# Kernel optimization log

Measured on AMD Instinct MI355X. Metric: run time of the kernel, lower is better.

The kernel has to match this reference:

```python
import jax, jax.numpy as jnp
import numpy as np

HEADS, DIM_HEAD, LANDMARKS, PINV_ITERS = 8, 64, 256, 6
CONV_K = 33  # nystrom residual depthwise conv kernel


def _pinv(x, iters):
    # Moore-Penrose iterative pseudo-inverse (lucidrains nystrom-attention)
    ax = jnp.abs(x)
    denom = ax.sum(-1).max() * ax.sum(-2).max()
    z = jnp.swapaxes(x, -1, -2) / denom
    I = jnp.eye(x.shape[-1], dtype=x.dtype)
    for _ in range(iters):
        xz = x @ z
        z = 0.25 * z @ (13.0 * I - xz @ (15.0 * I - xz @ (7.0 * I - xz)))
    return z


def _nystrom(x, qkv_w, out_w, out_b, conv_w):
    b, n, _ = x.shape
    m = LANDMARKS
    pad = (m - n % m) % m
    x = jnp.pad(x, ((0, 0), (pad, 0), (0, 0)))  # pad at front, as in reference impl
    npad = n + pad
    qkv = x @ qkv_w  # (b, npad, 3*h*dh), no bias
    q, k, v = jnp.split(qkv, 3, axis=-1)
    heads = lambda t: t.reshape(b, npad, HEADS, DIM_HEAD).transpose(0, 2, 1, 3)  # bhnd
    q, k, v = heads(q), heads(k), heads(v)
    q = q * (DIM_HEAD ** -0.5)
    l = npad // m
    q_l = q.reshape(b, HEADS, m, l, DIM_HEAD).mean(3)  # (b,h,m,dh) landmarks
    k_l = k.reshape(b, HEADS, m, l, DIM_HEAD).mean(3)
    attn1 = jax.nn.softmax(jnp.einsum('bhid,bhjd->bhij', q, k_l), -1)    # (b,h,npad,m)
    attn2 = jax.nn.softmax(jnp.einsum('bhid,bhjd->bhij', q_l, k_l), -1)  # (b,h,m,m)
    attn3 = jax.nn.softmax(jnp.einsum('bhid,bhjd->bhij', q_l, k), -1)    # (b,h,m,npad)
    out = (attn1 @ _pinv(attn2, PINV_ITERS)) @ (attn3 @ v)               # (b,h,npad,dh)
    # residual depthwise conv along sequence dim (groups=heads)
    res = jax.lax.conv_general_dilated(
        v, conv_w, (1, 1), ((CONV_K // 2, CONV_K // 2), (0, 0)),
        dimension_numbers=('NCHW', 'OIHW', 'NCHW'), feature_group_count=HEADS)
    out = out + res
    out = out.transpose(0, 2, 1, 3).reshape(b, npad, HEADS * DIM_HEAD)
    out = out @ out_w + out_b
    return out[:, -n:]  # drop front padding


def setup_inputs() -> dict:
    key = jax.random.key(0)
    ks = jax.random.split(key, 12)
    N, D, E, WP = 30000, 1024, 480000, 256
    inner = HEADS * DIM_HEAD
    s = lambda k, shape, fan: jax.random.normal(k, shape, jnp.float32) * (fan ** -0.5)
    return {
        'dense': jax.random.normal(ks[0], (1, N, D), jnp.float32),
        'edge_index': jax.random.randint(ks[1], (2, E), 0, N),
        'adj_vals': jax.random.uniform(ks[2], (E,), jnp.float32),
        'qkv_w': s(ks[3], (D, 3 * inner), D),
        'out_w': s(ks[4], (inner, D), inner),
        'out_b': jnp.zeros((D,), jnp.float32),
        'conv_w': s(ks[5], (HEADS, 1, CONV_K, 1), CONV_K),
        'wq_w': s(ks[6], (D, WP), D),
        'wq_b': jnp.zeros((WP,), jnp.float32),
        'wk_w': s(ks[7], (D, WP), D),
        'wk_b': jnp.zeros((WP,), jnp.float32),
        'wv_w': s(ks[8], (D, D), D),
        'wv_b': jnp.zeros((D,), jnp.float32),
    }


def reference(dense, edge_index, adj_vals, qkv_w, out_w, out_b, conv_w,
              wq_w, wq_b, wk_w, wk_b, wv_w, wv_b):
    n = dense.shape[1]
    enc = _nystrom(dense, qkv_w, out_w, out_b, conv_w)  # (1, n, D)
    encoder_output = enc[0] + dense                     # (1, n, D), broadcast as in torch
    x = encoder_output[0]                               # (n, D)
    # CustomAttention: per-edge dot-product scores
    q = x @ wq_w + wq_b                                 # (n, 256)
    k = x @ wk_w + wk_b
    scores = jnp.sum(q[edge_index[0]] * k[edge_index[1]], axis=-1) / jnp.sqrt(jnp.float32(q.shape[-1]))
    # NeighborAggregator: elementwise sparse mult by adjacency values, row-sum, global softmax
    A_raw = jax.ops.segment_sum(scores * adj_vals, edge_index[0], num_segments=n)  # (n,)
    norm_alpha = jax.nn.softmax(A_raw)
    value = dense @ wv_w + wv_b                         # (1, n, D)
    xl = norm_alpha[:, None] * value                    # (1, n, D)
    sw = jax.nn.sigmoid(-xl) ** 2
    xo = xl * 2.0 * sw + 2.0 * encoder_output * (1.0 - sw)
    return xo, A_raw
```

## Files before the change

### kernel.cpp

```cpp
#include <hip/hip_runtime.h>

#define NSEQ   30000
#define NPAD   30208
#define FPAD   208
#define DMODEL 1024
#define NHEAD  8
#define DHEAD  64
#define LM     256
#define LCHUNK 118
#define INNER  512
#define NCHUNK 59

typedef long long ll;
typedef unsigned short us;
typedef unsigned int uint32;
typedef __attribute__((ext_vector_type(8))) __bf16 bf16x8;
typedef __attribute__((ext_vector_type(4))) float f32x4;

__device__ __forceinline__ float b2f(us u) {
    union { unsigned int i; float f; } x; x.i = ((unsigned int)u) << 16; return x.f;
}
__device__ __forceinline__ us f2b(float f) {
    union { float f; unsigned int i; } x; x.f = f;
    unsigned int r = x.i + 0x7fffu + ((x.i >> 16) & 1u);
    return (us)(r >> 16);
}
__device__ __forceinline__ void gload16(const us* g, us* l) {
    __builtin_amdgcn_global_load_lds(
        (__attribute__((address_space(1))) void*)(const_cast<us*>(g)),
        (__attribute__((address_space(3))) void*)l, 16, 0, 0);
}

template<int EPI>
__global__ __launch_bounds__(256)
void bgemm(const us* __restrict__ A, const us* __restrict__ Bt,
           float* __restrict__ C, us* __restrict__ C2,
           const float* __restrict__ bias, const float* __restrict__ addp,
           int Mm, int Nn, int Kk, int lda, int ldb, int ldc, int ldadd,
           int Mstore, int Nstore, int rSub)
{
    __shared__ us As[2][128 * 32];
    __shared__ us Bs[2][128 * 32];

    int nwg = gridDim.x * gridDim.y;
    int orig = blockIdx.y * gridDim.x + blockIdx.x;
    int qd = nwg >> 3, rm = nwg & 7;
    int xcd = orig & 7, off = orig >> 3;
    int swz = (xcd < rm ? xcd * (qd + 1) : rm * (qd + 1) + (xcd - rm) * qd) + off;
    int by = swz / gridDim.x, bx = swz - by * gridDim.x;
    int m0 = by * 128, n0 = bx * 128;

    int tid = threadIdx.x, w = tid >> 6, lane = tid & 63;
    int wr = w >> 1, wc = w & 1;
    int nkt = Kk >> 5;

    int q0 = w * 128;
    int qa0 = q0 + lane, qa1 = q0 + 64 + lane;
    int r0s = qa0 >> 2, c0s = (qa0 & 3) ^ ((r0s >> 1) & 3);
    int r1s = qa1 >> 2, c1s = (qa1 & 3) ^ ((r1s >> 1) & 3);
    int ar0 = m0 + r0s; if (ar0 > Mm - 1) ar0 = Mm - 1;
    int ar1 = m0 + r1s; if (ar1 > Mm - 1) ar1 = Mm - 1;
    int br0 = n0 + r0s; if (br0 > Nn - 1) br0 = Nn - 1;
    int br1 = n0 + r1s; if (br1 > Nn - 1) br1 = Nn - 1;
    const us* pa0 = A + (ll)ar0 * lda + c0s * 8;
    const us* pa1 = A + (ll)ar1 * lda + c1s * 8;
    const us* pb0 = Bt + (ll)br0 * ldb + c0s * 8;
    const us* pb1 = Bt + (ll)br1 * ldb + c1s * 8;
    int la0o = q0 * 8, la1o = (q0 + 64) * 8;

    int l15 = lane & 15, l4 = lane >> 4;
    int aoff[4], boff[4];
#pragma unroll
    for (int f = 0; f < 4; f++) {
        int row = wr * 64 + f * 16 + l15;
        aoff[f] = row * 32 + ((l4 ^ ((row >> 1) & 3)) << 3);
        int col = wc * 64 + f * 16 + l15;
        boff[f] = col * 32 + ((l4 ^ ((col >> 1) & 3)) << 3);
    }

    f32x4 acc[4][4];
#pragma unroll
    for (int i = 0; i < 4; i++)
#pragma unroll
        for (int j = 0; j < 4; j++) acc[i][j] = (f32x4){0.f, 0.f, 0.f, 0.f};

    auto stage = [&](int buf, int kt) {
        int k0 = kt << 5;
        gload16(pa0 + k0, &As[buf][la0o]);
        gload16(pa1 + k0, &As[buf][la1o]);
        gload16(pb0 + k0, &Bs[buf][la0o]);
        gload16(pb1 + k0, &Bs[buf][la1o]);
    };

    stage(0, 0);
    for (int kt = 0; kt < nkt; ++kt) {
        int cur = kt & 1;
        if (kt + 1 < nkt) {
            stage(cur ^ 1, kt + 1);
            asm volatile("s_waitcnt vmcnt(4)" ::: "memory");
        } else {
            asm volatile("s_waitcnt vmcnt(0)" ::: "memory");
        }
        __builtin_amdgcn_s_barrier();
        asm volatile("" ::: "memory");
        bf16x8 af[4], bfr[4];
#pragma unroll
        for (int f = 0; f < 4; f++) af[f] = *(const bf16x8*)&As[cur][aoff[f]];
#pragma unroll
        for (int f = 0; f < 4; f++) bfr[f] = *(const bf16x8*)&Bs[cur][boff[f]];
#pragma unroll
        for (int i = 0; i < 4; i++)
#pragma unroll
            for (int j = 0; j < 4; j++)
                acc[i][j] = __builtin_amdgcn_mfma_f32_16x16x32_bf16(af[i], bfr[j], acc[i][j], 0, 0, 0);
        asm volatile("" ::: "memory");
        __builtin_amdgcn_s_barrier();
        asm volatile("" ::: "memory");
    }

#pragma unroll
    for (int fm = 0; fm < 4; fm++) {
        int rb = m0 + wr * 64 + fm * 16 + l4 * 4;
#pragma unroll
        for (int fn = 0; fn < 4; fn++) {
            int c = n0 + wc * 64 + fn * 16 + l15;
            if (c >= Nstore) continue;
#pragma unroll
            for (int i = 0; i < 4; i++) {
                int r = rb + i - rSub;
                if (r < 0 || r >= Mstore) continue;
                float v = acc[fm][fn][i];
                if (EPI == 3) {
                    int part = c >> 9, hh = (c >> 6) & 7, dd = c & 63;
                    float o = (part == 0) ? v * 0.125f : v;
                    C2[((ll)(part * 8 + hh) * NPAD + r) * 64 + dd] = f2b(o);
                } else if (EPI == 10) {
                    C2[(ll)r * ldc + c] = f2b(v + bias[c]);
                } else if (EPI == 12) {
                    C2[(ll)r * ldc + c] = f2b(v + bias[c] + addp[(ll)r * ldadd + c]);
                }
            }
        }
    }
}

__global__ __launch_bounds__(512)
void mega1(const us* __restrict__ XN, us* __restrict__ ZN, us* __restrict__ ZT,
           us* __restrict__ ZN2, us* __restrict__ ZT2,
           us* __restrict__ Y, us* __restrict__ W1T, us* __restrict__ W2T,
           us* __restrict__ W3T,
           const us* __restrict__ QLB, const us* __restrict__ Kh,
           const us* __restrict__ VT, us* __restrict__ KVPb, float* __restrict__ ZP,
           const us* __restrict__ Vh, const float* __restrict__ cw,
           us* __restrict__ ATTP,
           const us* __restrict__ DENSEP, const us* __restrict__ WVT,
           const float* __restrict__ wvb, us* __restrict__ VALB,
           const us* __restrict__ Qh, const us* __restrict__ KLB,
           us* __restrict__ P1)
{
    __shared__ us LDSu[24576];
    int b = blockIdx.x;
    int tid = threadIdx.x, w = tid >> 6, lane = tid & 63;
    int l15 = lane & 15, l4 = lane >> 4;

    if (b < 8) {
        __builtin_amdgcn_s_setprio(1);
        ll hb = (ll)b << 16;
        int wr = w >> 2, wc = w & 3;
        int sra = tid >> 2, sca = ((tid & 3) ^ ((sra >> 1) & 3)) * 8;
        int q1 = tid + 512;
        int srb1 = q1 >> 2, scb1 = ((q1 & 3) ^ ((srb1 >> 1) & 3)) * 8;
        int aoff[4], boff[4];
#pragma unroll
        for (int f = 0; f < 4; f++) {
            int row = wr * 64 + f * 16 + l15;
            aoff[f] = row * 32 + ((l4 ^ ((row >> 1) & 3)) << 3);
            int col = wc * 64 + f * 16 + l15;
            boff[f] = 4096 + col * 32 + ((l4 ^ ((col >> 1) & 3)) << 3);
        }
        f32x4 acc[4][4];
        auto gemmS = [&](const us* Ah, const us* Bt) {
#pragma unroll
            for (int i = 0; i < 4; i++)
#pragma unroll
                for (int j = 0; j < 4; j++) acc[i][j] = (f32x4){0.f, 0.f, 0.f, 0.f};
            const us* pa  = Ah + (ll)sra * 256 + sca;
            const us* pb0 = Bt + (ll)sra * 256 + sca;
            const us* pb1 = Bt + (ll)srb1 * 256 + scb1;
            auto stg = [&](int buf, int kt) {
                int k0 = kt << 5;
                gload16(pa + k0, &LDSu[buf + tid * 8]);
                gload16(pb0 + k0, &LDSu[buf + 4096 + tid * 8]);
                gload16(pb1 + k0, &LDSu[buf + 8192 + tid * 8]);
            };
            stg(0, 0);
            for (int kt = 0; kt < 8; ++kt) {
                int buf = (kt & 1) * 12288;
                if (kt < 7) {
                    stg(buf ^ 12288, kt + 1);
                    asm volatile("s_waitcnt vmcnt(3)" ::: "memory");
                } else {
                    asm volatile("s_waitcnt vmcnt(0)" ::: "memory");
                }
                __builtin_amdgcn_s_barrier();
                asm volatile("" ::: "memory");
                bf16x8 af[4], bfr[4];
#pragma unroll
                for (int f = 0; f < 4; f++) af[f] = *(const bf16x8*)&LDSu[buf + aoff[f]];
#pragma unroll
                for (int f = 0; f < 4; f++) bfr[f] = *(const bf16x8*)&LDSu[buf + boff[f]];
#pragma unroll
                for (int i = 0; i < 4; i++)
#pragma unroll
                    for (int j = 0; j < 4; j++)
                        acc[i][j] = __builtin_amdgcn_mfma_f32_16x16x32_bf16(af[i], bfr[j], acc[i][j], 0, 0, 0);
                asm volatile("" ::: "memory");
                __builtin_amdgcn_s_barrier();
                asm volatile("" ::: "memory");
            }
        };

        us* znc = ZN; us* ztc = ZT; us* znn = ZN2; us* ztn = ZT2;
        for (int it = 0; it < 6; ++it) {
#pragma unroll
            for (int hf = 0; hf < 2; ++hf) {
                gemmS(XN + hb + hf * 32768, ztc + hb);
#pragma unroll
                for (int fm = 0; fm < 4; fm++) {
                    int rb = hf * 128 + wr * 64 + fm * 16 + l4 * 4;
#pragma unroll
                    for (int fn = 0; fn < 4; fn++) {
                        int c = wc * 64 + fn * 16 + l15;
                        ushort4 u;
#pragma unroll
                        for (int i = 0; i < 4; i++) {
                            float v = acc[fm][fn][i];
                            Y[hb + (ll)(rb + i) * 256 + c] = f2b(v);
                            ((us*)&u)[i] = f2b(((rb + i == c) ? 7.0f : 0.0f) - v);
                        }
                        *(ushort4*)&W1T[hb + (ll)c * 256 + rb] = u;
                    }
                }
            }
            __syncthreads();
#pragma unroll
            for (int hf = 0; hf < 2; ++hf) {
                gemmS(Y + hb + hf * 32768, W1T + hb);
#pragma unroll
                for (int fm = 0; fm < 4; fm++) {
                    int rb = hf * 128 + wr * 64 + fm * 16 + l4 * 4;
#pragma unroll
                    for (int fn = 0; fn < 4; fn++) {
                        int c = wc * 64 + fn * 16 + l15;
                        ushort4 u;
#pragma unroll
                        for (int i = 0; i < 4; i++)
                            ((us*)&u)[i] = f2b(((rb + i == c) ? 15.0f : 0.0f) - acc[fm][fn][i]);
                        *(ushort4*)&W2T[hb + (ll)c * 256 + rb] = u;
                    }
                }
            }
            __syncthreads();
#pragma unroll
            for (int hf = 0; hf < 2; ++hf) {
                gemmS(Y + hb + hf * 32768, W2T + hb);
#pragma unroll
                for (int fm = 0; fm < 4; fm++) {
                    int rb = hf * 128 + wr * 64 + fm * 16 + l4 * 4;
#pragma unroll
                    for (int fn = 0; fn < 4; fn++) {
                        int c = wc * 64 + fn * 16 + l15;
                        ushort4 u;
#pragma unroll
                        for (int i = 0; i < 4; i++)
                            ((us*)&u)[i] = f2b(((rb + i == c) ? 13.0f : 0.0f) - acc[fm][fn][i]);
                        *(ushort4*)&W3T[hb + (ll)c * 256 + rb] = u;
                    }
                }
            }
            __syncthreads();
#pragma unroll
            for (int hf = 0; hf < 2; ++hf) {
                gemmS(znc + hb + hf * 32768, W3T + hb);
#pragma unroll
                for (int fm = 0; fm < 4; fm++) {
                    int rb = hf * 128 + wr * 64 + fm * 16 + l4 * 4;
#pragma unroll
                    for (int fn = 0; fn < 4; fn++) {
                        int c = wc * 64 + fn * 16 + l15;
                        ushort4 u;
#pragma unroll
                        for (int i = 0; i < 4; i++) {
                            us q = f2b(0.25f * acc[fm][fn][i]);
                            znn[hb + (ll)(rb + i) * 256 + c] = q;
                            ((us*)&u)[i] = q;
                        }
                        *(ushort4*)&ztn[hb + (ll)c * 256 + rb] = u;
                    }
                }
            }
            __syncthreads();
            us* tp;
            tp = znc; znc = znn; znn = tp;
            tp = ztc; ztc = ztn; ztn = tp;
        }
    } else if (b < 480) {
        if (w >= 4) return;
        int idx = b - 8;
        int h = idx & 7, chunk = idx >> 3;
        int c0 = chunk * 512;
        const us* QLh = QLB + (ll)h * 16384;
        const us* Khh = Kh + (ll)h * NPAD * 64;
        const us* VTh = VT + (ll)h * 64 * NPAD;
        us* P = &LDSu[w * 4096];

        bf16x8 aq[4][2];
#pragma unroll
        for (int fm = 0; fm < 4; fm++)
#pragma unroll
            for (int ks = 0; ks < 2; ks++)
                aq[fm][ks] = *(const bf16x8*)&QLh[(w * 64 + fm * 16 + l15) * 64 + l4 * 8 + ks * 32];

        f32x4 acc2[4][4];
        float zacc[4][4];
#pragma unroll
        for (int a = 0; a < 4; a++)
#pragma unroll
            for (int bb = 0; bb < 4; bb++) { acc2[a][bb] = (f32x4){0.f,0.f,0.f,0.f}; zacc[a][bb] = 0.f; }

        for (int sub = 0; sub < 8; ++sub) {
            int s0 = c0 + sub * 64;
            f32x4 s[4][4];
#pragma unroll
            for (int a = 0; a < 4; a++)
#pragma unroll
                for (int bb = 0; bb < 4; bb++) s[a][bb] = (f32x4){0.f,0.f,0.f,0.f};
#pragma unroll
            for (int ks = 0; ks < 2; ks++) {
                bf16x8 bk[4];
#pragma unroll
                for (int fn = 0; fn < 4; fn++)
                    bk[fn] = *(const bf16x8*)&Khh[(ll)(s0 + fn * 16 + l15) * 64 + l4 * 8 + ks * 32];
#pragma unroll
                for (int fm = 0; fm < 4; fm++)
#pragma unroll
                    for (int fn = 0; fn < 4; fn++)
                        s[fm][fn] = __builtin_amdgcn_mfma_f32_16x16x32_bf16(aq[fm][ks], bk[fn], s[fm][fn], 0, 0, 0);
            }
#pragma unroll
            for (int fm = 0; fm < 4; fm++)
#pragma unroll
                for (int i = 0; i < 4; i++) {
                    int row = fm * 16 + l4 * 4 + i;
#pragma unroll
                    for (int fn = 0; fn < 4; fn++) {
                        float e = __expf(s[fm][fn][i]);
                        zacc[fm][i] += e;
                        int col = fn * 16 + l15;
                        P[row * 64 + (((col >> 3) ^ (row & 7)) << 3) + (col & 7)] = f2b(e);
                    }
                }
#pragma unroll
            for (int ks = 0; ks < 2; ks++) {
                bf16x8 ap[4], bv[4];
#pragma unroll
                for (int fm = 0; fm < 4; fm++) {
                    int row = fm * 16 + l15;
                    int ch = (l4 + ks * 4) ^ (row & 7);
                    ap[fm] = *(const bf16x8*)&P[row * 64 + ch * 8];
                }
#pragma unroll
                for (int fn = 0; fn < 4; fn++)
                    bv[fn] = *(const bf16x8*)&VTh[(ll)(fn * 16 + l15) * NPAD + s0 + l4 * 8 + ks * 32];
#pragma unroll
                for (int fm = 0; fm < 4; fm++)
#pragma unroll
                    for (int fn = 0; fn < 4; fn++)
                        acc2[fm][fn] = __builtin_amdgcn_mfma_f32_16x16x32_bf16(ap[fm], bv[fn], acc2[fm][fn], 0, 0, 0);
            }
        }
        us* KP = KVPb + ((ll)h * NCHUNK + chunk) * 16384;
#pragma unroll
        for (int fm = 0; fm < 4; fm++)
#pragma unroll
            for (int fn = 0; fn < 4; fn++)
#pragma unroll
                for (int i = 0; i < 4; i++)
                    KP[(w * 64 + fm * 16 + l4 * 4 + i) * 64 + fn * 16 + l15] = f2b(acc2[fm][fn][i]);
#pragma unroll
        for (int fm = 0; fm < 4; fm++)
#pragma unroll
            for (int i = 0; i < 4; i++) {
                float zz = zacc[fm][i];
                zz += __shfl_xor(zz, 1, 64); zz += __shfl_xor(zz, 2, 64);
                zz += __shfl_xor(zz, 4, 64); zz += __shfl_xor(zz, 8, 64);
                if (l15 == 0)
                    ZP[((ll)h * NCHUNK + chunk) * 256 + w * 64 + fm * 16 + l4 * 4 + i] = zz;
            }
    } else if (b < 2360) {
        int vb = b - 480;
        int bx = vb & 7, by = vb >> 3;
        int m0 = by * 128, n0 = bx * 128;
        int wr = w >> 2, wc = w & 3;
        int sra = tid >> 2, sca = ((tid & 3) ^ ((sra >> 1) & 3)) * 8;
        int grow = m0 + sra; if (grow > NSEQ - 1) grow = NSEQ - 1;
        const us* pa = DENSEP + (ll)(grow + FPAD) * 1024 + sca;
        const us* pb = WVT + (ll)(n0 + sra) * 1024 + sca;
        int aoff[4], boff[2];
#pragma unroll
        for (int f = 0; f < 4; f++) {
            int row = wr * 64 + f * 16 + l15;
            aoff[f] = row * 32 + ((l4 ^ ((row >> 1) & 3)) << 3);
        }
#pragma unroll
        for (int f = 0; f < 2; f++) {
            int col = wc * 32 + f * 16 + l15;
            boff[f] = 4096 + col * 32 + ((l4 ^ ((col >> 1) & 3)) << 3);
        }
        f32x4 acc[4][2];
#pragma unroll
        for (int i = 0; i < 4; i++)
#pragma unroll
            for (int j = 0; j < 2; j++) acc[i][j] = (f32x4){0.f, 0.f, 0.f, 0.f};

        auto stg = [&](int buf, int kt) {
            int k0 = kt << 5;
            gload16(pa + k0, &LDSu[buf + tid * 8]);
            gload16(pb + k0, &LDSu[buf + 4096 + tid * 8]);
        };
        stg(0, 0);
        for (int kt = 0; kt < 32; ++kt) {
            int buf = (kt & 1) << 13;
            if (kt < 31) {
                stg(buf ^ 8192, kt + 1);
                asm volatile("s_waitcnt vmcnt(2)" ::: "memory");
            } else {
                asm volatile("s_waitcnt vmcnt(0)" ::: "memory");
            }
            __builtin_amdgcn_s_barrier();
            asm volatile("" ::: "memory");
            bf16x8 af[4], bfr[2];
#pragma unroll
            for (int f = 0; f < 4; f++) af[f] = *(const bf16x8*)&LDSu[buf + aoff[f]];
#pragma unroll
            for (int f = 0; f < 2; f++) bfr[f] = *(const bf16x8*)&LDSu[buf + boff[f]];
#pragma unroll
            for (int i = 0; i < 4; i++)
#pragma unroll
                for (int j = 0; j < 2; j++)
                    acc[i][j] = __builtin_amdgcn_mfma_f32_16x16x32_bf16(af[i], bfr[j], acc[i][j], 0, 0, 0);
            asm volatile("" ::: "memory");
            __builtin_amdgcn_s_barrier();
            asm volatile("" ::: "memory");
        }
#pragma unroll
        for (int fm = 0; fm < 4; fm++) {
            int rb = m0 + wr * 64 + fm * 16 + l4 * 4;
#pragma unroll
            for (int fn = 0; fn < 2; fn++) {
                int c = n0 + wc * 32 + fn * 16 + l15;
                float bias = wvb[c];
#pragma unroll
                for (int i = 0; i < 4; i++) {
                    int r = rb + i;
                    if (r < NSEQ) VALB[(ll)r * 1024 + c] = f2b(acc[fm][fn][i] + bias);
                }
            }
        }
    } else if (b < 4248) {
        int idx = b - 2360;
        int h = idx & 7, rc = idx >> 3;
        int rb0 = rc * 128 + w * 16;
        const us* Qhh = Qh + (ll)h * NPAD * 64;
        const us* KLh = KLB + (ll)h * 16384;
        us* P1h = P1 + (ll)h * NPAD * 256;

        int ra = rb0 + l15; if (ra > NSEQ - 1) ra = NSEQ - 1;
        bf16x8 aq0 = *(const bf16x8*)&Qhh[(ll)(ra + FPAD) * 64 + l4 * 8];
        bf16x8 aq1 = *(const bf16x8*)&Qhh[(ll)(ra + FPAD) * 64 + l4 * 8 + 32];

        f32x4 s[16];
#pragma unroll
        for (int fn = 0; fn < 16; fn++) s[fn] = (f32x4){0.f,0.f,0.f,0.f};
#pragma unroll
        for (int fn = 0; fn < 16; fn++) {
            bf16x8 bk0 = *(const bf16x8*)&KLh[(fn * 16 + l15) * 64 + l4 * 8];
            bf16x8 bk1 = *(const bf16x8*)&KLh[(fn * 16 + l15) * 64 + l4 * 8 + 32];
            s[fn] = __builtin_amdgcn_mfma_f32_16x16x32_bf16(aq0, bk0, s[fn], 0, 0, 0);
            s[fn] = __builtin_amdgcn_mfma_f32_16x16x32_bf16(aq1, bk1, s[fn], 0, 0, 0);
        }
#pragma unroll
        for (int i = 0; i < 4; i++) {
            float m = s[0][i];
#pragma unroll
            for (int fn = 1; fn < 16; fn++) m = fmaxf(m, s[fn][i]);
            m = fmaxf(m, __shfl_xor(m, 1, 64)); m = fmaxf(m, __shfl_xor(m, 2, 64));
            m = fmaxf(m, __shfl_xor(m, 4, 64)); m = fmaxf(m, __shfl_xor(m, 8, 64));
            float sum = 0.f;
#pragma unroll
            for (int fn = 0; fn < 16; fn++) {
                float e = __expf(s[fn][i] - m);
                s[fn][i] = e; sum += e;
            }
            sum += __shfl_xor(sum, 1, 64); sum += __shfl_xor(sum, 2, 64);
            sum += __shfl_xor(sum, 4, 64); sum += __shfl_xor(sum, 8, 64);
            float rinv = 1.0f / sum;
#pragma unroll
            for (int fn = 0; fn < 16; fn++) s[fn][i] *= rinv;
        }
#pragma unroll
        for (int i = 0; i < 4; i++) {
            int r = rb0 + l4 * 4 + i;
            if (r < NSEQ) {
#pragma unroll
                for (int fn = 0; fn < 16; fn++)
                    P1h[(ll)r * 256 + fn * 16 + l15] = f2b(s[fn][i]);
            }
        }
    } else {
        int cc = b - 4248;
        int h = cc & 7, ig = cc >> 3;
        int i = ig * 16 + w * 2 + (lane >> 5);
        int d0 = (lane & 31) * 2;
        if (i >= NSEQ) return;
        const us* Vh2 = Vh + (ll)h * NPAD * 64;
        int n0 = FPAD + i - 16;
        float s0 = 0.f, s1 = 0.f;
#pragma unroll
        for (int kk = 0; kk < 33; ++kk) {
            int n = n0 + kk;
            if (n < NPAD) {
                float wgt = cw[h * 33 + kk];
                uint32 v2 = *(const uint32*)&Vh2[(ll)n * 64 + d0];
                s0 = fmaf(wgt, b2f((us)(v2 & 0xffff)), s0);
                s1 = fmaf(wgt, b2f((us)(v2 >> 16)), s1);
            }
        }
        uint32 o = (uint32)f2b(s0) | ((uint32)f2b(s1) << 16);
        *(uint32*)&ATTP[(ll)i * INNER + h * 64 + d0] = o;
    }
}

#define BM 128
#define BN 64
#define BK 16
template<int TB, int EPI>
__global__ __launch_bounds__(256)
void gemm_k(const float* __restrict__ A, const float* __restrict__ B, float* __restrict__ C,
            int Mm, int Nn, int Kk, int lda, int ldb, int ldc,
            ll sA, ll sB, ll sC, float alpha, float diagv)
{
    __shared__ float As[BK][132];
    __shared__ float Bs[BK][68];
    int batch = blockIdx.z;
    A += (ll)batch * sA; B += (ll)batch * sB; C += (ll)batch * sC;
    int m0 = blockIdx.y * BM, n0 = blockIdx.x * BN;
    int tid = threadIdx.x, tx = tid & 15, ty = tid >> 4;
    int arow_t = tid >> 1, akh = (tid & 1) * 8;
    bool avalid = (m0 + arow_t < Mm);
    const float* Arow = A + (ll)(m0 + arow_t) * lda;
    float acc[8][4];
#pragma unroll
    for (int i = 0; i < 8; i++)
#pragma unroll
        for (int j = 0; j < 4; j++) acc[i][j] = 0.f;
    for (int kt = 0; kt < Kk / BK; ++kt) {
        int k0 = kt * BK;
        float4 av0 = make_float4(0, 0, 0, 0), av1 = av0;
        if (avalid) {
            av0 = *(const float4*)(Arow + k0 + akh);
            av1 = *(const float4*)(Arow + k0 + akh + 4);
        }
        float4 bv;
        if (TB == 0) bv = *(const float4*)(B + (ll)(k0 + (tid >> 4)) * ldb + n0 + (tid & 15) * 4);
        else         bv = *(const float4*)(B + (ll)(n0 + (tid >> 2)) * ldb + k0 + (tid & 3) * 4);
        __syncthreads();
        As[akh + 0][arow_t] = av0.x; As[akh + 1][arow_t] = av0.y;
        As[akh + 2][arow_t] = av0.z; As[akh + 3][arow_t] = av0.w;
        As[akh + 4][arow_t] = av1.x; As[akh + 5][arow_t] = av1.y;
        As[akh + 6][arow_t] = av1.z; As[akh + 7][arow_t] = av1.w;
        if (TB == 0) *(float4*)&Bs[tid >> 4][(tid & 15) * 4] = bv;
        else {
            int bk4 = (tid & 3) * 4, bn = tid >> 2;
            Bs[bk4 + 0][bn] = bv.x; Bs[bk4 + 1][bn] = bv.y;
            Bs[bk4 + 2][bn] = bv.z; Bs[bk4 + 3][bn] = bv.w;
        }
        __syncthreads();
#pragma unroll
        for (int kk = 0; kk < BK; kk++) {
            float ar[8], br[4];
            *(float4*)&ar[0] = *(const float4*)&As[kk][ty * 8];
            *(float4*)&ar[4] = *(const float4*)&As[kk][ty * 8 + 4];
            *(float4*)&br[0] = *(const float4*)&Bs[kk][tx * 4];
#pragma unroll
            for (int i = 0; i < 8; i++)
#pragma unroll
                for (int j = 0; j < 4; j++) acc[i][j] = fmaf(ar[i], br[j], acc[i][j]);
        }
    }
    int c0 = n0 + tx * 4;
#pragma unroll
    for (int i = 0; i < 8; i++) {
        int r = m0 + ty * 8 + i;
        if (r >= Mm) continue;
#pragma unroll
        for (int j = 0; j < 4; j++) {
            int c = c0 + j;
            if (c >= Nn) continue;
            if (EPI == 0) C[(ll)r * ldc + c] = alpha * acc[i][j];
        }
    }
}

__global__ void kv_reduce2(const us* __restrict__ KVPb, const float* __restrict__ ZP,
                           float* __restrict__ KV)
{
    int e = blockIdx.x * 256 + threadIdx.x;
    int h = e >> 14, r = (e >> 6) & 255;
    float s = 0.f, z = 0.f;
    for (int c = 0; c < NCHUNK; ++c) {
        s += b2f(KVPb[((ll)h * NCHUNK + c) * 16384 + (e & 16383)]);
        z += ZP[((ll)h * NCHUNK + c) * 256 + r];
    }
    KV[e] = s / z;
}

__global__ __launch_bounds__(256)
void pw_fused(const us* __restrict__ ZN, const float* __restrict__ KV,
              us* __restrict__ PWT)
{
    __shared__ us KT[64 * 264];
    int h = blockIdx.x;
    int tid = threadIdx.x, w = tid >> 6, lane = tid & 63;
    int l15 = lane & 15, l4 = lane >> 4;
    const float* KVh = KV + (ll)h * 16384;
#pragma unroll
    for (int i = 0; i < 64; ++i) {
        int idx = i * 256 + tid;
        int r = idx >> 6, c = idx & 63;
        KT[c * 264 + r] = f2b(KVh[idx]);
    }
    __syncthreads();
    const us* Zh = ZN + ((ll)h << 16);
    f32x4 acc[4][4];
#pragma unroll
    for (int i = 0; i < 4; i++)
#pragma unroll
        for (int j = 0; j < 4; j++) acc[i][j] = (f32x4){0.f, 0.f, 0.f, 0.f};
    int rw = w * 64;
    for (int ks = 0; ks < 8; ++ks) {
        int k0 = ks * 32 + l4 * 8;
        bf16x8 af[4], bfr[4];
#pragma unroll
        for (int f = 0; f < 4; f++)
            af[f] = *(const bf16x8*)&Zh[(ll)(rw + f * 16 + l15) * 256 + k0];
#pragma unroll
        for (int f = 0; f < 4; f++)
            bfr[f] = *(const bf16x8*)&KT[(f * 16 + l15) * 264 + k0];
#pragma unroll
        for (int i = 0; i < 4; i++)
#pragma unroll
            for (int j = 0; j < 4; j++)
                acc[i][j] = __builtin_amdgcn_mfma_f32_16x16x32_bf16(af[i], bfr[j], acc[i][j], 0, 0, 0);
    }
    us* PWh = PWT + (ll)h * 16384;
#pragma unroll
    for (int fm = 0; fm < 4; fm++)
#pragma unroll
        for (int fn = 0; fn < 4; fn++)
#pragma unroll
            for (int i = 0; i < 4; i++) {
                int r = rw + fm * 16 + l4 * 4 + i;
                int c = fn * 16 + l15;
                PWh[c * 256 + r] = f2b(acc[fm][fn][i]);
            }
}

__global__ __launch_bounds__(256)
void attn1_pv(const us* __restrict__ P1, const us* __restrict__ PWT,
              us* __restrict__ ATTP)
{
    int h = blockIdx.y, r0 = blockIdx.x * 128;
    int w = threadIdx.x >> 6, lane = threadIdx.x & 63;
    int l15 = lane & 15, l4 = lane >> 4;
    const us* P1h = P1 + (ll)h * NPAD * 256;
    const us* PWh = PWT + (ll)h * 16384;

    int ra[2];
#pragma unroll
    for (int fm = 0; fm < 2; fm++) {
        int r = r0 + w * 32 + fm * 16 + l15;
        ra[fm] = (r > NSEQ - 1) ? (NSEQ - 1) : r;
// ... 167 lines not shown
    if (i < n) p[i] = 0.f;
}

__global__ void edge_scores_b(const int* __restrict__ ei, const float* __restrict__ adj,
                              const us* __restrict__ qk2, float* __restrict__ Araw, int E)
{
    int gw = (blockIdx.x * 256 + threadIdx.x) >> 6;
    int lane = threadIdx.x & 63;
    if (gw >= E) return;
    int src = ei[gw], dst = ei[E + gw];
    const uint32* qp = (const uint32*)(qk2 + (ll)src * 512);
    const uint32* kp = (const uint32*)(qk2 + (ll)dst * 512 + 256);
    float acc = 0.f;
#pragma unroll
    for (int t = 0; t < 2; t++) {
        uint32 qu = qp[lane + t * 64], ku = kp[lane + t * 64];
        acc += b2f((us)(qu & 0xffff)) * b2f((us)(ku & 0xffff));
        acc += b2f((us)(qu >> 16)) * b2f((us)(ku >> 16));
    }
#pragma unroll
    for (int m = 32; m >= 1; m >>= 1) acc += __shfl_xor(acc, m, 64);
    if (lane == 0) atomicAdd(Araw + src, acc * adj[gw] * 0.0625f);
}

__global__ void softmax30k_stats(const float* __restrict__ A, float* __restrict__ scal)
{
    __shared__ float red[1024];
    int t = threadIdx.x;
    float m = -3.0e38f;
    for (int i = t; i < NSEQ; i += 1024) m = fmaxf(m, A[i]);
    red[t] = m; __syncthreads();
    for (int s = 512; s > 0; s >>= 1) { if (t < s) red[t] = fmaxf(red[t], red[t + s]); __syncthreads(); }
    m = red[0]; __syncthreads();
    float sum = 0.f;
    for (int i = t; i < NSEQ; i += 1024) sum += expf(A[i] - m);
    red[t] = sum; __syncthreads();
    for (int s = 512; s > 0; s >>= 1) { if (t < s) red[t] += red[t + s]; __syncthreads(); }
    if (t == 0) { scal[1] = m; scal[2] = red[0]; }
}

__global__ void alpha_kernel(const float* __restrict__ A, const float* __restrict__ scal,
                             float* __restrict__ alpha)
{
    int i = blockIdx.x * 256 + threadIdx.x;
    if (i < NSEQ) alpha[i] = expf(A[i] - scal[1]) / scal[2];
}

__global__ void gate_kernel(const float* __restrict__ alpha, const us* __restrict__ VALB,
                            const us* __restrict__ ENCB, float* __restrict__ OUT)
{
    ll e4 = ((ll)blockIdx.x * 256 + threadIdx.x) * 4;
    int i = (int)(e4 >> 10);
    float a = alpha[i];
    ushort4 vv = *(const ushort4*)&VALB[e4];
    ushort4 ee = *(const ushort4*)&ENCB[e4];
    float4 o;
    float* op = &o.x;
    const us* vp = (const us*)&vv;
    const us* ep = (const us*)&ee;
#pragma unroll
    for (int j = 0; j < 4; j++) {
        float xl = a * b2f(vp[j]);
        float sg = 1.0f / (1.0f + __expf(xl));
        float sw = sg * sg;
        op[j] = xl * 2.0f * sw + 2.0f * b2f(ep[j]) * (1.0f - sw);
    }
    *(float4*)&OUT[e4] = o;
}

extern "C" void kernel_launch(void* const* d_in, const int* in_sizes, int n_in,
                              void* d_out, int out_size, void* d_ws, size_t ws_size,
                              hipStream_t stream)
{
    const float* dense  = (const float*)d_in[0];
    const int*   ei     = (const int*)d_in[1];
    const float* adj    = (const float*)d_in[2];
    const float* qkv_w  = (const float*)d_in[3];
    const float* out_w  = (const float*)d_in[4];
    const float* out_b  = (const float*)d_in[5];
    const float* conv_w = (const float*)d_in[6];
    const float* wq_w   = (const float*)d_in[7];
    const float* wq_b   = (const float*)d_in[8];
    const float* wk_w   = (const float*)d_in[9];
    const float* wk_b   = (const float*)d_in[10];
    const float* wv_w   = (const float*)d_in[11];
    const float* wv_b   = (const float*)d_in[12];
    int E = in_sizes[2];

    char* w = (char*)d_ws;
    auto alloc = [&](ll bytes) { char* p = w; w += (bytes + 255) & ~(ll)255; return p; };

    us*    DENSEP = (us*)alloc((ll)NPAD * 1024 * 2);
    us*    QKVH   = (us*)alloc((ll)3 * 8 * NPAD * 64 * 2);
    us*    ENCB   = QKVH;
    us*    Qh = QKVH, *Kh = QKVH + (ll)8 * NPAD * 64, *Vh = QKVH + (ll)16 * NPAD * 64;
    us*    VT     = (us*)alloc((ll)8 * 64 * NPAD * 2);
    us*    QKVWT  = (us*)alloc((ll)1536 * 1024 * 2);
    us*    OUTWT  = (us*)alloc((ll)1024 * 512 * 2);
    us*    WQKT   = (us*)alloc((ll)512 * 1024 * 2);
    us*    WVT    = (us*)alloc((ll)1024 * 1024 * 2);
    float* WQKB   = (float*)alloc(512 * 4);
    float* QL     = (float*)alloc((ll)8 * 256 * 64 * 4);
    float* KL     = (float*)alloc((ll)8 * 256 * 64 * 4);
    us*    QLB    = (us*)alloc((ll)8 * 256 * 64 * 2);
    us*    KLB    = (us*)alloc((ll)8 * 256 * 64 * 2);
    float* A2     = (float*)alloc((ll)8 * 65536 * 4);
    us*    XN     = (us*)alloc((ll)8 * 65536 * 2);
    us*    ZN     = (us*)alloc((ll)8 * 65536 * 2);
    us*    ZT     = (us*)alloc((ll)8 * 65536 * 2);
    us*    ZN2    = (us*)alloc((ll)8 * 65536 * 2);
    us*    ZT2    = (us*)alloc((ll)8 * 65536 * 2);
    us*    Ybuf   = (us*)alloc((ll)8 * 65536 * 2);
    us*    W1T    = (us*)alloc((ll)8 * 65536 * 2);
    us*    W2T    = (us*)alloc((ll)8 * 65536 * 2);
    us*    W3T    = (us*)alloc((ll)8 * 65536 * 2);
    us*    KVPb   = (us*)alloc((ll)8 * NCHUNK * 16384 * 2);
    float* ZP     = (float*)alloc((ll)8 * NCHUNK * 256 * 4);
    float* KV     = (float*)alloc((ll)8 * 16384 * 4);
    us*    PWT    = (us*)alloc((ll)8 * 16384 * 2);
    float* HM     = (float*)alloc(64 * 4);
    float* SC     = (float*)alloc(64 * 4);
    float* ALPHA  = (float*)alloc(30000 * 4);
    us*    ATTP   = (us*)alloc((ll)NSEQ * 512 * 2);
    us*    QK2B   = ATTP;
    us*    VALB   = (us*)alloc((ll)NSEQ * 1024 * 2);
    us*    P1     = (us*)alloc((ll)8 * NPAD * 256 * 2);

    float* OUT  = (float*)d_out;
    float* ARAW = OUT + (ll)NSEQ * DMODEL;

    trans_f2b<<<dim3(48, 32, 1), 256, 0, stream>>>(qkv_w, QKVWT, 1024, 1536, 0, 0);
    trans_f2b<<<dim3(32, 16, 1), 256, 0, stream>>>(out_w, OUTWT, 512, 1024, 0, 0);
    trans_f2b<<<dim3(8, 32, 1), 256, 0, stream>>>(wq_w, WQKT, 1024, 256, 0, 0);
    trans_f2b<<<dim3(8, 32, 1), 256, 0, stream>>>(wk_w, WQKT + (ll)256 * 1024, 1024, 256, 0, 0);
    trans_f2b<<<dim3(32, 32, 1), 256, 0, stream>>>(wv_w, WVT, 1024, 1024, 0, 0);
    concat_bias<<<1, 256, 0, stream>>>(wq_b, wk_b, WQKB);
    dense_pad_b<<<NPAD, 256, 0, stream>>>(dense, DENSEP);

    bgemm<3><<<dim3(12, 236, 1), 256, 0, stream>>>(DENSEP, QKVWT, nullptr, QKVH,
        nullptr, nullptr, NPAD, 1536, 1024, 1024, 1024, 0, 0, NPAD, 1536, 0);

    landmark_mean_b<<<2048, 64, 0, stream>>>(Qh, QL, QLB);
    landmark_mean_b<<<2048, 64, 0, stream>>>(Kh, KL, KLB);

    gemm_k<1, 0><<<dim3(4, 2, 8), 256, 0, stream>>>(QL, KL, A2, LM, LM, DHEAD,
        DHEAD, DHEAD, LM, LM * DHEAD, LM * DHEAD, LM * LM, 1.f, 0.f);
    rowsoftmax256<<<2048, 256, 0, stream>>>(A2);
    colrow_max<<<8, 256, 0, stream>>>(A2, HM);
    denom_fin<<<1, 1, 0, stream>>>(HM, SC);
    pinv_init<<<2048, 256, 0, stream>>>(A2, SC, XN, ZN, ZT);

    trans_b2b<<<dim3(2, 944, 8), 256, 0, stream>>>(Vh, VT, NPAD, 64, (ll)NPAD * 64, (ll)64 * NPAD);

    mega1<<<19248, 512, 0, stream>>>(XN, ZN, ZT, ZN2, ZT2, Ybuf, W1T, W2T, W3T,
                                     QLB, Kh, VT, KVPb, ZP, Vh, conv_w, ATTP,
                                     DENSEP, WVT, wv_b, VALB, Qh, KLB, P1);

    kv_reduce2<<<512, 256, 0, stream>>>(KVPb, ZP, KV);
    pw_fused<<<8, 256, 0, stream>>>(ZN, KV, PWT);

    attn1_pv<<<dim3(235, 8), 256, 0, stream>>>(P1, PWT, ATTP);

    bgemm<12><<<dim3(8, 235, 1), 256, 0, stream>>>(ATTP, OUTWT, nullptr, ENCB,
        out_b, dense, NSEQ, 1024, 512, 512, 512, 1024, 1024, NSEQ, 1024, 0);

    bgemm<10><<<dim3(4, 235, 1), 256, 0, stream>>>(ENCB, WQKT, nullptr, QK2B,
        WQKB, nullptr, NSEQ, 512, 1024, 1024, 1024, 512, 0, NSEQ, 512, 0);

    zero_f32<<<(NSEQ + 255) / 256, 256, 0, stream>>>(ARAW, NSEQ);
    edge_scores_b<<<(E + 3) / 4, 256, 0, stream>>>(ei, adj, QK2B, ARAW, E);
    softmax30k_stats<<<1, 1024, 0, stream>>>(ARAW, SC);
    alpha_kernel<<<(NSEQ + 255) / 256, 256, 0, stream>>>(ARAW, SC, ALPHA);

    gate_kernel<<<30000, 256, 0, stream>>>(ALPHA, VALB, ENCB, OUT);
}
```

Before: 1.352 ms.

## Convert mega1 side tasks into persistent work loop over fixed grid

The mega kernel used to launch 19248 blocks, one per task. It now launches 256 blocks: 8 handle the pinv iterations and 248 persistent workers stride over a combined task list of attn3, value GEMM, P1 softmax and conv tasks. The attn3 task now uses all 8 waves by processing two head/chunk pairs per block, with a smaller LDS P buffer. Each conv task covers 64 rows instead of 16. This cuts block launch overhead and idle waves, at the risk of load imbalance and of the pinv blocks no longer overlapping with as many concurrent blocks.

New measurement: 1.546 ms. 1.14x slower.

```diff
diff --git a/kernel.cpp b/kernel.cpp
--- a/kernel.cpp
+++ b/kernel.cpp
@@ -10,6 +10,13 @@
 #define LCHUNK 118
 #define INNER  512
 #define NCHUNK 59
+
+#define NWORK     248
+#define T_ATTN3   236
+#define T_VAL     1880
+#define T_P1      1888
+#define T_CONV    3752
+#define T_TOTAL   (T_ATTN3 + T_VAL + T_P1 + T_CONV)
 
 typedef long long ll;
 typedef unsigned short us;
@@ -304,240 +311,251 @@
             tp = znc; znc = znn; znn = tp;
             tp = ztc; ztc = ztn; ztn = tp;
         }
-    } else if (b < 480) {
-        if (w >= 4) return;
-        int idx = b - 8;
-        int h = idx & 7, chunk = idx >> 3;
-        int c0 = chunk * 512;
-        const us* QLh = QLB + (ll)h * 16384;
-        const us* Khh = Kh + (ll)h * NPAD * 64;
-        const us* VTh = VT + (ll)h * 64 * NPAD;
-        us* P = &LDSu[w * 4096];
-
-        bf16x8 aq[4][2];
-#pragma unroll
-        for (int fm = 0; fm < 4; fm++)
-#pragma unroll
-            for (int ks = 0; ks < 2; ks++)
-                aq[fm][ks] = *(const bf16x8*)&QLh[(w * 64 + fm * 16 + l15) * 64 + l4 * 8 + ks * 32];
-
-        f32x4 acc2[4][4];
-        float zacc[4][4];
-#pragma unroll
-        for (int a = 0; a < 4; a++)
-#pragma unroll
-            for (int bb = 0; bb < 4; bb++) { acc2[a][bb] = (f32x4){0.f,0.f,0.f,0.f}; zacc[a][bb] = 0.f; }
-
-        for (int sub = 0; sub < 8; ++sub) {
-            int s0 = c0 + sub * 64;
-            f32x4 s[4][4];
+        return;
+    }
+
+    for (int t = b - 8; t < T_TOTAL; t += NWORK) {
+        __syncthreads();
+        if (t < T_ATTN3) {
+            int cid2 = t * 2 + (w >> 2);
+            int h = cid2 & 7, chunk = cid2 >> 3;
+            int ws = w & 3;
+            int c0 = chunk * 512;
+            const us* QLh = QLB + (ll)h * 16384;
+            const us* Khh = Kh + (ll)h * NPAD * 64;
+            const us* VTh = VT + (ll)h * 64 * NPAD;
+            us* P = &LDSu[w * 2048];
+
+            bf16x8 aq[4][2];
+#pragma unroll
+            for (int fm = 0; fm < 4; fm++)
+#pragma unroll
+                for (int ks = 0; ks < 2; ks++)
+                    aq[fm][ks] = *(const bf16x8*)&QLh[(ws * 64 + fm * 16 + l15) * 64 + l4 * 8 + ks * 32];
+
+            f32x4 acc2[4][4];
+            float zacc[4][4];
 #pragma unroll
             for (int a = 0; a < 4; a++)
 #pragma unroll
-                for (int bb = 0; bb < 4; bb++) s[a][bb] = (f32x4){0.f,0.f,0.f,0.f};
-#pragma unroll
-            for (int ks = 0; ks < 2; ks++) {
-                bf16x8 bk[4];
+                for (int bb = 0; bb < 4; bb++) { acc2[a][bb] = (f32x4){0.f,0.f,0.f,0.f}; zacc[a][bb] = 0.f; }
+
+            for (int sub = 0; sub < 8; ++sub) {
+                int s0 = c0 + sub * 64;
+                f32x4 s[4][4];
+#pragma unroll
+                for (int a = 0; a < 4; a++)
+#pragma unroll
+                    for (int bb = 0; bb < 4; bb++) s[a][bb] = (f32x4){0.f,0.f,0.f,0.f};
+#pragma unroll
+                for (int ks = 0; ks < 2; ks++) {
+                    bf16x8 bk[4];
+#pragma unroll
+                    for (int fn = 0; fn < 4; fn++)
+                        bk[fn] = *(const bf16x8*)&Khh[(ll)(s0 + fn * 16 + l15) * 64 + l4 * 8 + ks * 32];
+#pragma unroll
+                    for (int fm = 0; fm < 4; fm++)
+#pragma unroll
+                        for (int fn = 0; fn < 4; fn++)
+                            s[fm][fn] = __builtin_amdgcn_mfma_f32_16x16x32_bf16(aq[fm][ks], bk[fn], s[fm][fn], 0, 0, 0);
+                }
+#pragma unroll
+                for (int fm = 0; fm < 4; fm++)
+#pragma unroll
+                    for (int i = 0; i < 4; i++) {
+                        int row = fm * 16 + l4 * 4 + i;
+#pragma unroll
+                        for (int fn = 0; fn < 4; fn++) {
+                            float e = __expf(s[fm][fn][i]);
+                            zacc[fm][i] += e;
+                            int col = ((fn & 1) * 16 + l15);
+                            P[(row + (fn >> 1) * 64) * 16 + ((col >> 3) ^ (row & 3)) * 8 + (col & 7)] = f2b(e);
+                        }
+                    }
+#pragma unroll
+                for (int ks = 0; ks < 2; ks++) {
+                    bf16x8 ap[4], bv[4];
+#pragma unroll
+                    for (int fm = 0; fm < 4; fm++) {
+                        int row = fm * 16 + l15;
+                        int grp = (l4 + ks * 4);
+                        int half = grp >> 2, ch = grp & 3;
+                        ap[fm] = *(const bf16x8*)&P[(row + half * 64) * 16 + (ch ^ (row & 3)) * 8];
+                    }
+#pragma unroll
+                    for (int fn = 0; fn < 4; fn++)
+                        bv[fn] = *(const bf16x8*)&VTh[(ll)(fn * 16 + l15) * NPAD + s0 + l4 * 8 + ks * 32];
+#pragma unroll
+                    for (int fm = 0; fm < 4; fm++)
+#pragma unroll
+                        for (int fn = 0; fn < 4; fn++)
+                            acc2[fm][fn] = __builtin_amdgcn_mfma_f32_16x16x32_bf16(ap[fm], bv[fn], acc2[fm][fn], 0, 0, 0);
+                }
+            }
+            us* KP = KVPb + ((ll)h * NCHUNK + chunk) * 16384;
+#pragma unroll
+            for (int fm = 0; fm < 4; fm++)
 #pragma unroll
                 for (int fn = 0; fn < 4; fn++)
-                    bk[fn] = *(const bf16x8*)&Khh[(ll)(s0 + fn * 16 + l15) * 64 + l4 * 8 + ks * 32];
-#pragma unroll
-                for (int fm = 0; fm < 4; fm++)
-#pragma unroll
-                    for (int fn = 0; fn < 4; fn++)
-                        s[fm][fn] = __builtin_amdgcn_mfma_f32_16x16x32_bf16(aq[fm][ks], bk[fn], s[fm][fn], 0, 0, 0);
-            }
+#pragma unroll
+                    for (int i = 0; i < 4; i++)
+                        KP[(ws * 64 + fm * 16 + l4 * 4 + i) * 64 + fn * 16 + l15] = f2b(acc2[fm][fn][i]);
 #pragma unroll
             for (int fm = 0; fm < 4; fm++)
 #pragma unroll
                 for (int i = 0; i < 4; i++) {
-                    int row = fm * 16 + l4 * 4 + i;
-#pragma unroll
-                    for (int fn = 0; fn < 4; fn++) {
-                        float e = __expf(s[fm][fn][i]);
-                        zacc[fm][i] += e;
-                        int col = fn * 16 + l15;
-                        P[row * 64 + (((col >> 3) ^ (row & 7)) << 3) + (col & 7)] = f2b(e);
+                    float zz = zacc[fm][i];
+                    zz += __shfl_xor(zz, 1, 64); zz += __shfl_xor(zz, 2, 64);
+                    zz += __shfl_xor(zz, 4, 64); zz += __shfl_xor(zz, 8, 64);
+                    if (l15 == 0)
+                        ZP[((ll)h * NCHUNK + chunk) * 256 + ws * 64 + fm * 16 + l4 * 4 + i] = zz;
+                }
+        } else if (t < T_ATTN3 + T_VAL) {
+            int vb = t - T_ATTN3;
+            int bx = vb & 7, by = vb >> 3;
+            int m0 = by * 128, n0 = bx * 128;
+            int wr = w >> 2, wc = w & 3;
+            int sra = tid >> 2, sca = ((tid & 3) ^ ((sra >> 1) & 3)) * 8;
+            int grow = m0 + sra; if (grow > NSEQ - 1) grow = NSEQ - 1;
+            const us* pa = DENSEP + (ll)(grow + FPAD) * 1024 + sca;
+            const us* pb = WVT + (ll)(n0 + sra) * 1024 + sca;
+            int aoff[4], boff[2];
+#pragma unroll
+            for (int f = 0; f < 4; f++) {
+                int row = wr * 64 + f * 16 + l15;
+                aoff[f] = row * 32 + ((l4 ^ ((row >> 1) & 3)) << 3);
+            }
+#pragma unroll
+            for (int f = 0; f < 2; f++) {
+                int col = wc * 32 + f * 16 + l15;
+                boff[f] = 4096 + col * 32 + ((l4 ^ ((col >> 1) & 3)) << 3);
+            }
+            f32x4 acc[4][2];
+#pragma unroll
+            for (int i = 0; i < 4; i++)
+#pragma unroll
+                for (int j = 0; j < 2; j++) acc[i][j] = (f32x4){0.f, 0.f, 0.f, 0.f};
+
+            auto stg = [&](int buf, int kt) {
+                int k0 = kt << 5;
+                gload16(pa + k0, &LDSu[buf + tid * 8]);
+                gload16(pb + k0, &LDSu[buf + 4096 + tid * 8]);
+            };
+            stg(0, 0);
+            for (int kt = 0; kt < 32; ++kt) {
+                int buf = (kt & 1) << 13;
+                if (kt < 31) {
+                    stg(buf ^ 8192, kt + 1);
+                    asm volatile("s_waitcnt vmcnt(2)" ::: "memory");
+                } else {
+                    asm volatile("s_waitcnt vmcnt(0)" ::: "memory");
+                }
+                __builtin_amdgcn_s_barrier();
+                asm volatile("" ::: "memory");
+                bf16x8 af[4], bfr[2];
+#pragma unroll
+                for (int f = 0; f < 4; f++) af[f] = *(const bf16x8*)&LDSu[buf + aoff[f]];
+#pragma unroll
+                for (int f = 0; f < 2; f++) bfr[f] = *(const bf16x8*)&LDSu[buf + boff[f]];
+#pragma unroll
+                for (int i = 0; i < 4; i++)
+#pragma unroll
+                    for (int j = 0; j < 2; j++)
+                        acc[i][j] = __builtin_amdgcn_mfma_f32_16x16x32_bf16(af[i], bfr[j], acc[i][j], 0, 0, 0);
+                asm volatile("" ::: "memory");
+                __builtin_amdgcn_s_barrier();
+                asm volatile("" ::: "memory");
+            }
+#pragma unroll
+            for (int fm = 0; fm < 4; fm++) {
+                int rb = m0 + wr * 64 + fm * 16 + l4 * 4;
+#pragma unroll
+                for (int fn = 0; fn < 2; fn++) {
+                    int c = n0 + wc * 32 + fn * 16 + l15;
+                    float bias = wvb[c];
+#pragma unroll
+                    for (int i = 0; i < 4; i++) {
+                        int r = rb + i;
+                        if (r < NSEQ) VALB[(ll)r * 1024 + c] = f2b(acc[fm][fn][i] + bias);
                     }
                 }
-#pragma unroll
-            for (int ks = 0; ks < 2; ks++) {
-                bf16x8 ap[4], bv[4];
-#pragma unroll
-                for (int fm = 0; fm < 4; fm++) {
-                    int row = fm * 16 + l15;
-                    int ch = (l4 + ks * 4) ^ (row & 7);
-                    ap[fm] = *(const bf16x8*)&P[row * 64 + ch * 8];
-                }
-#pragma unroll
-                for (int fn = 0; fn < 4; fn++)
-                    bv[fn] = *(const bf16x8*)&VTh[(ll)(fn * 16 + l15) * NPAD + s0 + l4 * 8 + ks * 32];
-#pragma unroll
-                for (int fm = 0; fm < 4; fm++)
-#pragma unroll
-                    for (int fn = 0; fn < 4; fn++)
-                        acc2[fm][fn] = __builtin_amdgcn_mfma_f32_16x16x32_bf16(ap[fm], bv[fn], acc2[fm][fn], 0, 0, 0);
+            }
+        } else if (t < T_ATTN3 + T_VAL + T_P1) {
+            int idx = t - (T_ATTN3 + T_VAL);
+            int h = idx & 7, rc = idx >> 3;
+            int rb0 = rc * 128 + w * 16;
+            const us* Qhh = Qh + (ll)h * NPAD * 64;
+            const us* KLh = KLB + (ll)h * 16384;
+            us* P1h = P1 + (ll)h * NPAD * 256;
+
+            int ra = rb0 + l15; if (ra > NSEQ - 1) ra = NSEQ - 1;
+            bf16x8 aq0 = *(const bf16x8*)&Qhh[(ll)(ra + FPAD) * 64 + l4 * 8];
+            bf16x8 aq1 = *(const bf16x8*)&Qhh[(ll)(ra + FPAD) * 64 + l4 * 8 + 32];
+
+            f32x4 s[16];
+#pragma unroll
+            for (int fn = 0; fn < 16; fn++) s[fn] = (f32x4){0.f,0.f,0.f,0.f};
+#pragma unroll
+            for (int fn = 0; fn < 16; fn++) {
+                bf16x8 bk0 = *(const bf16x8*)&KLh[(fn * 16 + l15) * 64 + l4 * 8];
+                bf16x8 bk1 = *(const bf16x8*)&KLh[(fn * 16 + l15) * 64 + l4 * 8 + 32];
+                s[fn] = __builtin_amdgcn_mfma_f32_16x16x32_bf16(aq0, bk0, s[fn], 0, 0, 0);
+                s[fn] = __builtin_amdgcn_mfma_f32_16x16x32_bf16(aq1, bk1, s[fn], 0, 0, 0);
+            }
+#pragma unroll
+            for (int i = 0; i < 4; i++) {
+                float m = s[0][i];
+#pragma unroll
+                for (int fn = 1; fn < 16; fn++) m = fmaxf(m, s[fn][i]);
+                m = fmaxf(m, __shfl_xor(m, 1, 64)); m = fmaxf(m, __shfl_xor(m, 2, 64));
+                m = fmaxf(m, __shfl_xor(m, 4, 64)); m = fmaxf(m, __shfl_xor(m, 8, 64));
+                float sum = 0.f;
+#pragma unroll
+                for (int fn = 0; fn < 16; fn++) {
+                    float e = __expf(s[fn][i] - m);
+                    s[fn][i] = e; sum += e;
+                }
+                sum += __shfl_xor(sum, 1, 64); sum += __shfl_xor(sum, 2, 64);
+                sum += __shfl_xor(sum, 4, 64); sum += __shfl_xor(sum, 8, 64);
+                float rinv = 1.0f / sum;
+#pragma unroll
+                for (int fn = 0; fn < 16; fn++) s[fn][i] *= rinv;
+            }
+#pragma unroll
+            for (int i = 0; i < 4; i++) {
+                int r = rb0 + l4 * 4 + i;
+                if (r < NSEQ) {
+#pragma unroll
+                    for (int fn = 0; fn < 16; fn++)
+                        P1h[(ll)r * 256 + fn * 16 + l15] = f2b(s[fn][i]);
+                }
+            }
+        } else {
+            int task = t - (T_ATTN3 + T_VAL + T_P1);
+            int h = task & 7, ig = task >> 3;
+            const us* Vh2 = Vh + (ll)h * NPAD * 64;
+            int d0 = (lane & 31) * 2;
+#pragma unroll
+            for (int g = 0; g < 4; ++g) {
+                int i = ig * 64 + g * 16 + w * 2 + (lane >> 5);
+                if (i < NSEQ) {
+                    int n0 = FPAD + i - 16;
+                    float s0 = 0.f, s1 = 0.f;
+#pragma unroll
+                    for (int kk = 0; kk < 33; ++kk) {
+                        int n = n0 + kk;
+                        if (n < NPAD) {
+                            float wgt = cw[h * 33 + kk];
+                            uint32 v2 = *(const uint32*)&Vh2[(ll)n * 64 + d0];
+                            s0 = fmaf(wgt, b2f((us)(v2 & 0xffff)), s0);
+                            s1 = fmaf(wgt, b2f((us)(v2 >> 16)), s1);
+                        }
+                    }
+                    uint32 o = (uint32)f2b(s0) | ((uint32)f2b(s1) << 16);
+                    *(uint32*)&ATTP[(ll)i * INNER + h * 64 + d0] = o;
+                }
             }
         }
-        us* KP = KVPb + ((ll)h * NCHUNK + chunk) * 16384;
-#pragma unroll
-        for (int fm = 0; fm < 4; fm++)
-#pragma unroll
-            for (int fn = 0; fn < 4; fn++)
-#pragma unroll
-                for (int i = 0; i < 4; i++)
-                    KP[(w * 64 + fm * 16 + l4 * 4 + i) * 64 + fn * 16 + l15] = f2b(acc2[fm][fn][i]);
-#pragma unroll
-        for (int fm = 0; fm < 4; fm++)
-#pragma unroll
-            for (int i = 0; i < 4; i++) {
-                float zz = zacc[fm][i];
-                zz += __shfl_xor(zz, 1, 64); zz += __shfl_xor(zz, 2, 64);
-                zz += __shfl_xor(zz, 4, 64); zz += __shfl_xor(zz, 8, 64);
-                if (l15 == 0)
-                    ZP[((ll)h * NCHUNK + chunk) * 256 + w * 64 + fm * 16 + l4 * 4 + i] = zz;
-            }
-    } else if (b < 2360) {
-        int vb = b - 480;
-        int bx = vb & 7, by = vb >> 3;
-        int m0 = by * 128, n0 = bx * 128;
-        int wr = w >> 2, wc = w & 3;
-        int sra = tid >> 2, sca = ((tid & 3) ^ ((sra >> 1) & 3)) * 8;
-        int grow = m0 + sra; if (grow > NSEQ - 1) grow = NSEQ - 1;
-        const us* pa = DENSEP + (ll)(grow + FPAD) * 1024 + sca;
-        const us* pb = WVT + (ll)(n0 + sra) * 1024 + sca;
-        int aoff[4], boff[2];
-#pragma unroll
-        for (int f = 0; f < 4; f++) {
-            int row = wr * 64 + f * 16 + l15;
-            aoff[f] = row * 32 + ((l4 ^ ((row >> 1) & 3)) << 3);
-        }
-#pragma unroll
-        for (int f = 0; f < 2; f++) {
-            int col = wc * 32 + f * 16 + l15;
-            boff[f] = 4096 + col * 32 + ((l4 ^ ((col >> 1) & 3)) << 3);
-        }
-        f32x4 acc[4][2];
-#pragma unroll
-        for (int i = 0; i < 4; i++)
-#pragma unroll
-            for (int j = 0; j < 2; j++) acc[i][j] = (f32x4){0.f, 0.f, 0.f, 0.f};
-
-        auto stg = [&](int buf, int kt) {
-            int k0 = kt << 5;
-            gload16(pa + k0, &LDSu[buf + tid * 8]);
-            gload16(pb + k0, &LDSu[buf + 4096 + tid * 8]);
-        };
-        stg(0, 0);
-        for (int kt = 0; kt < 32; ++kt) {
-            int buf = (kt & 1) << 13;
-            if (kt < 31) {
-                stg(buf ^ 8192, kt + 1);
-                asm volatile("s_waitcnt vmcnt(2)" ::: "memory");
-            } else {
-                asm volatile("s_waitcnt vmcnt(0)" ::: "memory");
-            }
-            __builtin_amdgcn_s_barrier();
-            asm volatile("" ::: "memory");
-            bf16x8 af[4], bfr[2];
-#pragma unroll
-            for (int f = 0; f < 4; f++) af[f] = *(const bf16x8*)&LDSu[buf + aoff[f]];
-#pragma unroll
-            for (int f = 0; f < 2; f++) bfr[f] = *(const bf16x8*)&LDSu[buf + boff[f]];
-#pragma unroll
-            for (int i = 0; i < 4; i++)
-#pragma unroll
-                for (int j = 0; j < 2; j++)
-                    acc[i][j] = __builtin_amdgcn_mfma_f32_16x16x32_bf16(af[i], bfr[j], acc[i][j], 0, 0, 0);
-            asm volatile("" ::: "memory");
-            __builtin_amdgcn_s_barrier();
-            asm volatile("" ::: "memory");
-        }
-#pragma unroll
-        for (int fm = 0; fm < 4; fm++) {
-            int rb = m0 + wr * 64 + fm * 16 + l4 * 4;
-#pragma unroll
-            for (int fn = 0; fn < 2; fn++) {
-                int c = n0 + wc * 32 + fn * 16 + l15;
-                float bias = wvb[c];
-#pragma unroll
-                for (int i = 0; i < 4; i++) {
-                    int r = rb + i;
-                    if (r < NSEQ) VALB[(ll)r * 1024 + c] = f2b(acc[fm][fn][i] + bias);
-                }
-            }
-        }
-    } else if (b < 4248) {
-        int idx = b - 2360;
-        int h = idx & 7, rc = idx >> 3;
-        int rb0 = rc * 128 + w * 16;
-        const us* Qhh = Qh + (ll)h * NPAD * 64;
-        const us* KLh = KLB + (ll)h * 16384;
-        us* P1h = P1 + (ll)h * NPAD * 256;
-
-        int ra = rb0 + l15; if (ra > NSEQ - 1) ra = NSEQ - 1;
-        bf16x8 aq0 = *(const bf16x8*)&Qhh[(ll)(ra + FPAD) * 64 + l4 * 8];
-        bf16x8 aq1 = *(const bf16x8*)&Qhh[(ll)(ra + FPAD) * 64 + l4 * 8 + 32];
-
-        f32x4 s[16];
-#pragma unroll
-        for (int fn = 0; fn < 16; fn++) s[fn] = (f32x4){0.f,0.f,0.f,0.f};
-#pragma unroll
-        for (int fn = 0; fn < 16; fn++) {
-            bf16x8 bk0 = *(const bf16x8*)&KLh[(fn * 16 + l15) * 64 + l4 * 8];
-            bf16x8 bk1 = *(const bf16x8*)&KLh[(fn * 16 + l15) * 64 + l4 * 8 + 32];
-            s[fn] = __builtin_amdgcn_mfma_f32_16x16x32_bf16(aq0, bk0, s[fn], 0, 0, 0);
-            s[fn] = __builtin_amdgcn_mfma_f32_16x16x32_bf16(aq1, bk1, s[fn], 0, 0, 0);
-        }
-#pragma unroll
-        for (int i = 0; i < 4; i++) {
-            float m = s[0][i];
-#pragma unroll
-            for (int fn = 1; fn < 16; fn++) m = fmaxf(m, s[fn][i]);
-            m = fmaxf(m, __shfl_xor(m, 1, 64)); m = fmaxf(m, __shfl_xor(m, 2, 64));
-            m = fmaxf(m, __shfl_xor(m, 4, 64)); m = fmaxf(m, __shfl_xor(m, 8, 64));
-            float sum = 0.f;
-#pragma unroll
-            for (int fn = 0; fn < 16; fn++) {
-                float e = __expf(s[fn][i] - m);
-                s[fn][i] = e; sum += e;
-            }
-            sum += __shfl_xor(sum, 1, 64); sum += __shfl_xor(sum, 2, 64);
-            sum += __shfl_xor(sum, 4, 64); sum += __shfl_xor(sum, 8, 64);
-            float rinv = 1.0f / sum;
-#pragma unroll
-            for (int fn = 0; fn < 16; fn++) s[fn][i] *= rinv;
-        }
-#pragma unroll
-        for (int i = 0; i < 4; i++) {
-            int r = rb0 + l4 * 4 + i;
-            if (r < NSEQ) {
-#pragma unroll
-                for (int fn = 0; fn < 16; fn++)
-                    P1h[(ll)r * 256 + fn * 16 + l15] = f2b(s[fn][i]);
-            }
-        }
-    } else {
-        int cc = b - 4248;
-        int h = cc & 7, ig = cc >> 3;
-        int i = ig * 16 + w * 2 + (lane >> 5);
-        int d0 = (lane & 31) * 2;
-        if (i >= NSEQ) return;
-        const us* Vh2 = Vh + (ll)h * NPAD * 64;
-        int n0 = FPAD + i - 16;
-        float s0 = 0.f, s1 = 0.f;
-#pragma unroll
-        for (int kk = 0; kk < 33; ++kk) {
-            int n = n0 + kk;
-            if (n < NPAD) {
-                float wgt = cw[h * 33 + kk];
-                uint32 v2 = *(const uint32*)&Vh2[(ll)n * 64 + d0];
-                s0 = fmaf(wgt, b2f((us)(v2 & 0xffff)), s0);
-                s1 = fmaf(wgt, b2f((us)(v2 >> 16)), s1);
-            }
-        }
-        uint32 o = (uint32)f2b(s0) | ((uint32)f2b(s1) << 16);
-        *(uint32*)&ATTP[(ll)i * INNER + h * 64 + d0] = o;
     }
 }
 
@@ -1011,9 +1029,9 @@
 
     trans_b2b<<<dim3(2, 944, 8), 256, 0, stream>>>(Vh, VT, NPAD, 64, (ll)NPAD * 64, (ll)64 * NPAD);
 
-    mega1<<<19248, 512, 0, stream>>>(XN, ZN, ZT, ZN2, ZT2, Ybuf, W1T, W2T, W3T,
-                                     QLB, Kh, VT, KVPb, ZP, Vh, conv_w, ATTP,
-                                     DENSEP, WVT, wv_b, VALB, Qh, KLB, P1);
+    mega1<<<256, 512, 0, stream>>>(XN, ZN, ZT, ZN2, ZT2, Ybuf, W1T, W2T, W3T,
+                                   QLB, Kh, VT, KVPb, ZP, Vh, conv_w, ATTP,
+                                   DENSEP, WVT, wv_b, VALB, Qh, KLB, P1);
 
     kv_reduce2<<<512, 256, 0, stream>>>(KVPb, ZP, KV);
     pw_fused<<<8, 256, 0, stream>>>(ZN, KV, PWT);
```
